# Kernel optimization log

Hardware: AMD Instinct MI355X
Metric: run time of the kernel (lower is better)

Reference implementation:

```python
import jax, jax.numpy as jnp
import numpy as np

B, S, D, H = 4, 2048, 1024, 16
HS = D // H  # head_size = 64


def setup_inputs() -> dict:
    key = jax.random.key(0)
    ks = jax.random.split(key, 6)
    scale = 1.0 / np.sqrt(D)
    return {
        "x": jax.random.normal(ks[0], (B, S, D), dtype=jnp.float32),
        "Wk": jax.random.normal(ks[1], (D, D), dtype=jnp.float32) * scale,
        "Wq": jax.random.normal(ks[2], (D, D), dtype=jnp.float32) * scale,
        "Wv": jax.random.normal(ks[3], (D, D), dtype=jnp.float32) * scale,
        "Wo": jax.random.normal(ks[4], (D, D), dtype=jnp.float32) * scale,
        "bo": jnp.zeros((D,), dtype=jnp.float32),
    }


def reference(x, Wk, Wq, Wv, Wo, bo):
    b, s, d = x.shape
    # torch nn.Linear: y = x @ W.T
    def heads(W):
        return (x @ W.T).reshape(b, s, H, HS).transpose(0, 2, 1, 3)  # [b,h,s,hs]
    k, q, v = heads(Wk), heads(Wq), heads(Wv)
    att = jnp.einsum("bhqd,bhkd->bhqk", q, k) * (1.0 / np.sqrt(HS))
    causal = jnp.tril(jnp.ones((s, s), dtype=bool))
    att = jnp.where(causal, att, -jnp.inf)
    att = jax.nn.softmax(att, axis=-1)
    # dropout in eval mode (identity) for deterministic reference
    out = jnp.einsum("bhqk,bhkd->bhqd", att, v)  # [b,h,s,hs]
    out = out.transpose(0, 2, 1, 3).reshape(b, s, d)
    return out @ Wo.T + bo
```

## Files before the change

kernel.cpp:

```cpp
#include <hip/hip_runtime.h>

#define B_ 4
#define S_ 2048
#define D_ 1024
#define H_ 16
#define HS_ 64

typedef float f32x4 __attribute__((ext_vector_type(4)));
typedef short bf16x8 __attribute__((ext_vector_type(8)));

__device__ inline short f2bf(float f) {
  union { float f; unsigned u; } v; v.f = f;
  unsigned r = v.u + 0x7fffu + ((v.u >> 16) & 1u);
  return (short)(r >> 16);
}
__device__ inline unsigned fbits(float f) {
  union { float f; unsigned u; } v; v.f = f; return v.u;
}

__device__ inline void load_lds16(const short* g, short* l) {
  __builtin_amdgcn_global_load_lds((const __attribute__((address_space(1))) void*)g,
                                   (__attribute__((address_space(3))) void*)l, 16, 0, 0);
}

__global__ __launch_bounds__(256) void cvt_f32_bf16(const float* __restrict__ in,
                                                    short* __restrict__ out, int n) {
  const int i = (blockIdx.x * 256 + threadIdx.x) * 4;
  if (i < n) {
    const float4 v = *(const float4*)(in + i);
    short4 o;
    o.x = f2bf(v.x); o.y = f2bf(v.y); o.z = f2bf(v.z); o.w = f2bf(v.w);
    *(short4*)(out + i) = o;
  }
}

__global__ __launch_bounds__(256) void cvt4_f32_bf16(const float* __restrict__ w0, const float* __restrict__ w1,
                                                     const float* __restrict__ w2, const float* __restrict__ w3,
                                                     short* __restrict__ o0, short* __restrict__ o1,
                                                     short* __restrict__ o2, short* __restrict__ o3, int n) {
  const float* in; short* out;
  switch (blockIdx.y) {
    case 0: in = w0; out = o0; break;
    case 1: in = w1; out = o1; break;
    case 2: in = w2; out = o2; break;
    default: in = w3; out = o3; break;
  }
  const int i = (blockIdx.x * 256 + threadIdx.x) * 4;
  if (i < n) {
    const float4 v = *(const float4*)(in + i);
    short4 o;
    o.x = f2bf(v.x); o.y = f2bf(v.y); o.z = f2bf(v.z); o.w = f2bf(v.w);
    *(short4*)(out + i) = o;
  }
}

__device__ inline void mfma_core(const short* lA, const short* lB, int wm, int wn,
                                 int col, int quad, f32x4 acc[4][4]) {
  bf16x8 af[4], bfr[4];
  for (int i = 0; i < 4; i++) af[i]  = *(const bf16x8*)&lA[(wm + i * 16 + col) * 32 + quad * 8];
  for (int j = 0; j < 4; j++) bfr[j] = *(const bf16x8*)&lB[(wn + j * 16 + col) * 32 + quad * 8];
  for (int i = 0; i < 4; i++)
    for (int j = 0; j < 4; j++)
      acc[i][j] = __builtin_amdgcn_mfma_f32_16x16x32_bf16(af[i], bfr[j], acc[i][j], 0, 0, 0);
}

template <bool CF32>
__global__ __launch_bounds__(256) void gemm_bb(const short* __restrict__ A,
                                               const short* __restrict__ Bt,
                                               void* __restrict__ Cv,
                                               const float* __restrict__ bias,
                                               int M, int N, int K) {
  __shared__ __align__(16) short lA[128 * 32];
  __shared__ __align__(16) short lB[128 * 32];
  const int tid = threadIdx.x;
  const int wave = tid >> 6, lane = tid & 63;
  const int quad = lane >> 4, col = lane & 15;
  const int m0 = blockIdx.x * 128, n0 = blockIdx.y * 128;
  const int wm = (wave >> 1) * 64, wn = (wave & 1) * 64;
  const int srow = wave * 32 + (lane >> 2);
  const int scol = (lane & 3) * 8;

  f32x4 acc[4][4];
  for (int i = 0; i < 4; i++)
    for (int j = 0; j < 4; j++) acc[i][j] = (f32x4){0.f, 0.f, 0.f, 0.f};

  for (int k0 = 0; k0 < K; k0 += 32) {
    __syncthreads();
    load_lds16(&A[(size_t)(m0 + srow) * K + k0 + scol],       &lA[srow * 32 + scol]);
    load_lds16(&A[(size_t)(m0 + srow + 16) * K + k0 + scol],  &lA[(srow + 16) * 32 + scol]);
    load_lds16(&Bt[(size_t)(n0 + srow) * K + k0 + scol],      &lB[srow * 32 + scol]);
    load_lds16(&Bt[(size_t)(n0 + srow + 16) * K + k0 + scol], &lB[(srow + 16) * 32 + scol]);
    __syncthreads();
    mfma_core(lA, lB, wm, wn, col, quad, acc);
  }

  for (int j = 0; j < 4; j++) {
    const int gn = n0 + wn + j * 16 + col;
    const float bv = bias ? bias[gn] : 0.f;
    for (int i = 0; i < 4; i++) {
      const int gm = m0 + wm + i * 16 + quad * 4;
      for (int r = 0; r < 4; r++) {
        if (CF32) ((float*)Cv)[(size_t)(gm + r) * N + gn] = acc[i][j][r] + bv;
        else      ((short*)Cv)[(size_t)(gm + r) * N + gn] = f2bf(acc[i][j][r] + bv);
      }
    }
  }
}

__global__ __launch_bounds__(256) void gemm_qkv(const short* __restrict__ A,
                                                const short* Wq, const short* Wk, const short* Wv,
                                                short* Cq, short* Ck, short* Cvt) {
  __shared__ __align__(16) short lA[128 * 32];
  __shared__ __align__(16) short lB[128 * 32];
  const int nsel = blockIdx.y >> 3;
  const int n0 = (blockIdx.y & 7) * 128;
  const short* Bt = nsel == 0 ? Wq : (nsel == 1 ? Wk : Wv);
  const int tid = threadIdx.x;
  const int wave = tid >> 6, lane = tid & 63;
  const int quad = lane >> 4, col = lane & 15;
  const int m0 = blockIdx.x * 128;
  const int wm = (wave >> 1) * 64, wn = (wave & 1) * 64;
  const int srow = wave * 32 + (lane >> 2);
  const int scol = (lane & 3) * 8;
  const int K = D_, N = D_;

  f32x4 acc[4][4];
  for (int i = 0; i < 4; i++)
    for (int j = 0; j < 4; j++) acc[i][j] = (f32x4){0.f, 0.f, 0.f, 0.f};

  for (int k0 = 0; k0 < K; k0 += 32) {
    __syncthreads();
    load_lds16(&A[(size_t)(m0 + srow) * K + k0 + scol],       &lA[srow * 32 + scol]);
    load_lds16(&A[(size_t)(m0 + srow + 16) * K + k0 + scol],  &lA[(srow + 16) * 32 + scol]);
    load_lds16(&Bt[(size_t)(n0 + srow) * K + k0 + scol],      &lB[srow * 32 + scol]);
    load_lds16(&Bt[(size_t)(n0 + srow + 16) * K + k0 + scol], &lB[(srow + 16) * 32 + scol]);
    __syncthreads();
    mfma_core(lA, lB, wm, wn, col, quad, acc);
  }

  if (nsel < 2) {
    short* C = nsel ? Ck : Cq;
    const float sc = nsel == 0 ? 0.18033688f : 1.0f;
    for (int j = 0; j < 4; j++) {
      const int gn = n0 + wn + j * 16 + col;
      for (int i = 0; i < 4; i++) {
        const int gm = m0 + wm + i * 16 + quad * 4;
        for (int r = 0; r < 4; r++)
          C[(size_t)(gm + r) * N + gn] = f2bf(acc[i][j][r] * sc);
      }
    }
  } else {
    for (int j = 0; j < 4; j++) {
      const int gn = n0 + wn + j * 16 + col;
      for (int i = 0; i < 4; i++) {
        const int gm = m0 + wm + i * 16 + quad * 4;
        const int bb = gm >> 11, s = gm & 2047;
        short4 o;
        o.x = f2bf(acc[i][j][0]); o.y = f2bf(acc[i][j][1]);
        o.z = f2bf(acc[i][j][2]); o.w = f2bf(acc[i][j][3]);
        *(short4*)&Cvt[((size_t)bb * D_ + gn) * (size_t)S_ + s] = o;
      }
    }
  }
}

__global__ __launch_bounds__(256) void flash_attn6(const short* __restrict__ Q,
                                                   const short* __restrict__ Kt,
                                                   const short* __restrict__ Vt,
                                                   short* __restrict__ O) {
  __shared__ __align__(16) short lK[2][64 * 64];
  __shared__ __align__(16) short lV[2][64 * 64];
  __shared__ __align__(16) short pl[4][16 * 64];
  const int tid = threadIdx.x, wave = tid >> 6, lane = tid & 63;
  const int quad = lane >> 4, col = lane & 15;
  const int bh = blockIdx.x;
  const int b = bh >> 4, h = bh & 15;
  const size_t qkbase = (size_t)b * S_ * D_ + (size_t)h * HS_;
  const size_t vtbase = ((size_t)b * D_ + (size_t)h * HS_) * (size_t)S_;

  const int srow = tid >> 3;
  const int scg = (tid & 7) ^ (srow & 7);
  const int cs0 = (quad ^ (col & 7)) * 8;
  const int cs1 = ((quad + 4) ^ (col & 7)) * 8;
  short* plw = pl[wave];

  bf16x8 ones;
  for (int i = 0; i < 8; i++) ones[i] = (short)0x3F80;

  int nb = 0;

  for (int half = 0; half < 2; half++) {
    const int s = half ? (int)blockIdx.y : 31 - (int)blockIdx.y;
    const int qmin = s * 64 + wave * 16;
    const int L = s;

    load_lds16(&Kt[qkbase + (size_t)srow * D_ + scg * 8],        &lK[nb][tid * 8]);
    load_lds16(&Kt[qkbase + (size_t)(32 + srow) * D_ + scg * 8], &lK[nb][2048 + tid * 8]);
    load_lds16(&Vt[vtbase + (size_t)srow * S_ + scg * 8],        &lV[nb][tid * 8]);
    load_lds16(&Vt[vtbase + (size_t)(srow + 32) * S_ + scg * 8], &lV[nb][2048 + tid * 8]);
    const int cur0 = nb;
    nb ^= 1;

    bf16x8 qf[2];
    for (int x = 0; x < 2; x++)
      qf[x] = *(const bf16x8*)&Q[qkbase + (size_t)(qmin + col) * D_ + x * 32 + quad * 8];

    f32x4 oacc[4], lacc;
    for (int dt = 0; dt < 4; dt++) oacc[dt] = (f32x4){0.f, 0.f, 0.f, 0.f};
    lacc = (f32x4){0.f, 0.f, 0.f, 0.f};

    for (int nt = 0; nt <= L; nt++) {
      const int n0 = nt * 64;
      const int cur = cur0 ^ (nt & 1);
      __syncthreads();
      if (nt < L) {
        const int nn = n0 + 64;
        load_lds16(&Kt[qkbase + (size_t)(nn + srow) * D_ + scg * 8],      &lK[nb][tid * 8]);
        load_lds16(&Kt[qkbase + (size_t)(nn + 32 + srow) * D_ + scg * 8], &lK[nb][2048 + tid * 8]);
        load_lds16(&Vt[vtbase + (size_t)srow * S_ + nn + scg * 8],        &lV[nb][tid * 8]);
        load_lds16(&Vt[vtbase + (size_t)(srow + 32) * S_ + nn + scg * 8], &lV[nb][2048 + tid * 8]);
        nb ^= 1;
      }

      const short* lKc = lK[cur];
      const short* lVc = lV[cur];
      const bool needM = (nt == L);

      bf16x8 kf[4][2];
      for (int t = 0; t < 4; t++) {
        const int rb = (t * 16 + col) * 64;
        kf[t][0] = *(const bf16x8*)&lKc[rb + cs0];
        kf[t][1] = *(const bf16x8*)&lKc[rb + cs1];
      }

      const int qg = qmin + col;
      for (int t = 0; t < 4; t++) {
        f32x4 z = (f32x4){0.f, 0.f, 0.f, 0.f};
        __builtin_amdgcn_s_setprio(1);
        z = __builtin_amdgcn_mfma_f32_16x16x32_bf16(kf[t][0], qf[0], z, 0, 0, 0);
        z = __builtin_amdgcn_mfma_f32_16x16x32_bf16(kf[t][1], qf[1], z, 0, 0, 0);
        __builtin_amdgcn_s_setprio(0);
        float p0 = exp2f(z[0]);
        float p1 = exp2f(z[1]);
        float p2 = exp2f(z[2]);
        float p3 = exp2f(z[3]);
        if (needM) {
          const int kv = n0 + t * 16 + quad * 4;
          if (kv + 0 > qg) p0 = 0.f;
          if (kv + 1 > qg) p1 = 0.f;
          if (kv + 2 > qg) p2 = 0.f;
          if (kv + 3 > qg) p3 = 0.f;
        }
        unsigned d0 = __builtin_amdgcn_perm(fbits(p1), fbits(p0), 0x07060302u);
        unsigned d1 = __builtin_amdgcn_perm(fbits(p3), fbits(p2), 0x07060302u);
        const int cc = (2 * t + (quad >> 1)) ^ (col & 7);
        uint2 w; w.x = d0; w.y = d1;
        *(uint2*)&plw[col * 64 + cc * 8 + (quad & 1) * 4] = w;
      }

      for (int h2 = 0; h2 < 2; h2++) {
        const int cgo = ((h2 * 4 + quad) ^ (col & 7)) * 8;
        const bf16x8 pf = *(const bf16x8*)&plw[col * 64 + cgo];
        bf16x8 vf[4];
        for (int dt = 0; dt < 4; dt++)
          vf[dt] = *(const bf16x8*)&lVc[(dt * 16 + col) * 64 + cgo];
        __builtin_amdgcn_s_setprio(1);
        lacc = __builtin_amdgcn_mfma_f32_16x16x32_bf16(pf, ones, lacc, 0, 0, 0);
        for (int dt = 0; dt < 4; dt++)
          oacc[dt] = __builtin_amdgcn_mfma_f32_16x16x32_bf16(pf, vf[dt], oacc[dt], 0, 0, 0);
        __builtin_amdgcn_s_setprio(0);
      }
    }

    for (int r = 0; r < 4; r++) {
      const float inv = 1.f / lacc[r];
      const size_t row = qkbase + (size_t)(qmin + quad * 4 + r) * D_;
      for (int dt = 0; dt < 4; dt++)
        O[row + dt * 16 + col] = f2bf(oacc[dt][r] * inv);
    }
  }
}

__global__ __launch_bounds__(256) void gemm_ff(const float* __restrict__ A,
                                               const float* __restrict__ Bt,
                                               short* __restrict__ C,
                                               int M, int N, int K) {
  __shared__ __align__(16) short lA[128 * 32];
  __shared__ __align__(16) short lB[128 * 32];
  const int tid = threadIdx.x;
  const int wave = tid >> 6, lane = tid & 63;
  const int quad = lane >> 4, col = lane & 15;
  const int m0 = blockIdx.y * 128, n0 = blockIdx.x * 128;
  const int wm = (wave >> 1) * 64, wn = (wave & 1) * 64;
  const int srow2 = tid >> 1;
  const int sc = (tid & 1) * 16;

  f32x4 acc[4][4];
  for (int i = 0; i < 4; i++)
    for (int j = 0; j < 4; j++) acc[i][j] = (f32x4){0.f, 0.f, 0.f, 0.f};

  for (int k0 = 0; k0 < K; k0 += 32) {
    __syncthreads();
    {
      const float4* ga = (const float4*)&A[(size_t)(m0 + srow2) * K + k0 + sc];
      const float4 v0 = ga[0], v1 = ga[1], v2 = ga[2], v3 = ga[3];
      bf16x8 p0, p1;
      p0[0] = f2bf(v0.x); p0[1] = f2bf(v0.y); p0[2] = f2bf(v0.z); p0[3] = f2bf(v0.w);
      p0[4] = f2bf(v1.x); p0[5] = f2bf(v1.y); p0[6] = f2bf(v1.z); p0[7] = f2bf(v1.w);
      p1[0] = f2bf(v2.x); p1[1] = f2bf(v2.y); p1[2] = f2bf(v2.z); p1[3] = f2bf(v2.w);
      p1[4] = f2bf(v3.x); p1[5] = f2bf(v3.y); p1[6] = f2bf(v3.z); p1[7] = f2bf(v3.w);
      *(bf16x8*)&lA[srow2 * 32 + sc]     = p0;
      *(bf16x8*)&lA[srow2 * 32 + sc + 8] = p1;
    }
    {
      const float4* gb = (const float4*)&Bt[(size_t)(n0 + srow2) * K + k0 + sc];
      const float4 v0 = gb[0], v1 = gb[1], v2 = gb[2], v3 = gb[3];
      bf16x8 p0, p1;
      p0[0] = f2bf(v0.x); p0[1] = f2bf(v0.y); p0[2] = f2bf(v0.z); p0[3] = f2bf(v0.w);
      p0[4] = f2bf(v1.x); p0[5] = f2bf(v1.y); p0[6] = f2bf(v1.z); p0[7] = f2bf(v1.w);
      p1[0] = f2bf(v2.x); p1[1] = f2bf(v2.y); p1[2] = f2bf(v2.z); p1[3] = f2bf(v2.w);
      p1[4] = f2bf(v3.x); p1[5] = f2bf(v3.y); p1[6] = f2bf(v3.z); p1[7] = f2bf(v3.w);
      *(bf16x8*)&lB[srow2 * 32 + sc]     = p0;
      *(bf16x8*)&lB[srow2 * 32 + sc + 8] = p1;
    }
    __syncthreads();
    mfma_core(lA, lB, wm, wn, col, quad, acc);
  }

  for (int j = 0; j < 4; j++) {
    const int gn = n0 + wn + j * 16 + col;
    for (int i = 0; i < 4; i++) {
      const int gm = m0 + wm + i * 16 + quad * 4;
      for (int r = 0; r < 4; r++)
        C[(size_t)(gm + r) * N + gn] = f2bf(acc[i][j][r]);
    }
  }
}

__global__ __launch_bounds__(256) void gemm_out_bf(const short* __restrict__ A,
                                                   const float* __restrict__ Bt,
                                                   float* __restrict__ C,
                                                   const float* __restrict__ bias,
                                                   int M, int N, int K) {
  __shared__ __align__(16) short lA[128 * 32];
  __shared__ __align__(16) short lB[128 * 32];
  const int tid = threadIdx.x;
  const int wave = tid >> 6, lane = tid & 63;
  const int quad = lane >> 4, col = lane & 15;
  const int m0 = blockIdx.y * 128, n0 = blockIdx.x * 128;
  const int wm = (wave >> 1) * 64, wn = (wave & 1) * 64;
  const int srow = wave * 32 + (lane >> 2);
  const int scol = (lane & 3) * 8;
  const int srow2 = tid >> 1;
  const int sc = (tid & 1) * 16;

  f32x4 acc[4][4];
  for (int i = 0; i < 4; i++)
    for (int j = 0; j < 4; j++) acc[i][j] = (f32x4){0.f, 0.f, 0.f, 0.f};

  for (int k0 = 0; k0 < K; k0 += 32) {
    __syncthreads();
    load_lds16(&A[(size_t)(m0 + srow) * K + k0 + scol],      &lA[srow * 32 + scol]);
    load_lds16(&A[(size_t)(m0 + srow + 16) * K + k0 + scol], &lA[(srow + 16) * 32 + scol]);
    {
      const float4* gb = (const float4*)&Bt[(size_t)(n0 + srow2) * K + k0 + sc];
      const float4 v0 = gb[0], v1 = gb[1], v2 = gb[2], v3 = gb[3];
      bf16x8 p0, p1;
      p0[0] = f2bf(v0.x); p0[1] = f2bf(v0.y); p0[2] = f2bf(v0.z); p0[3] = f2bf(v0.w);
      p0[4] = f2bf(v1.x); p0[5] = f2bf(v1.y); p0[6] = f2bf(v1.z); p0[7] = f2bf(v1.w);
      p1[0] = f2bf(v2.x); p1[1] = f2bf(v2.y); p1[2] = f2bf(v2.z); p1[3] = f2bf(v2.w);
      p1[4] = f2bf(v3.x); p1[5] = f2bf(v3.y); p1[6] = f2bf(v3.z); p1[7] = f2bf(v3.w);
      *(bf16x8*)&lB[srow2 * 32 + sc]     = p0;
      *(bf16x8*)&lB[srow2 * 32 + sc + 8] = p1;
    }
    __syncthreads();
    mfma_core(lA, lB, wm, wn, col, quad, acc);
  }

  for (int j = 0; j < 4; j++) {
    const int gn = n0 + wn + j * 16 + col;
    const float bv = bias ? bias[gn] : 0.f;
    for (int i = 0; i < 4; i++) {
      const int gm = m0 + wm + i * 16 + quad * 4;
      for (int r = 0; r < 4; r++)
        C[(size_t)(gm + r) * N + gn] = acc[i][j][r] + bv;
    }
  }
}

__global__ __launch_bounds__(64) void flash_attn(const short* __restrict__ Q,
                                                 const short* __restrict__ K,
                                                 const short* __restrict__ V,
                                                 short* __restrict__ O) {
  __shared__ __align__(16) short pl[16 * 40];
  const int lane = threadIdx.x;
  const int quad = lane >> 4, col = lane & 15;
  const int blk = blockIdx.x;
  const int qt = blk & 127;
  const int bh = blk >> 7;
  const int b = bh >> 4, h = bh & 15;
  const int q0 = qt * 16;
  const size_t base = (size_t)b * S_ * D_ + (size_t)h * HS_;

  const bf16x8 qf0 = *(const bf16x8*)&Q[base + (size_t)(q0 + col) * D_ + quad * 8];
  const bf16x8 qf1 = *(const bf16x8*)&Q[base + (size_t)(q0 + col) * D_ + 32 + quad * 8];

  float mr[4], lr[4];
  f32x4 oacc[4];
  for (int r = 0; r < 4; r++) { mr[r] = -1e30f; lr[r] = 0.f; }
  for (int dt = 0; dt < 4; dt++) oacc[dt] = (f32x4){0.f, 0.f, 0.f, 0.f};

  const int ntiles = (q0 + 15) / 32 + 1;
  for (int nt = 0; nt < ntiles; nt++) {
    const int n0 = nt * 32;
    f32x4 s[2];
    s[0] = (f32x4){0.f, 0.f, 0.f, 0.f};
    s[1] = (f32x4){0.f, 0.f, 0.f, 0.f};
    for (int t = 0; t < 2; t++) {
      const short* kp = &K[base + (size_t)(n0 + t * 16 + col) * D_ + quad * 8];
      const bf16x8 kf0 = *(const bf16x8*)kp;
      const bf16x8 kf1 = *(const bf16x8*)(kp + 32);
      s[t] = __builtin_amdgcn_mfma_f32_16x16x32_bf16(qf0, kf0, s[t], 0, 0, 0);
      s[t] = __builtin_amdgcn_mfma_f32_16x16x32_bf16(qf1, kf1, s[t], 0, 0, 0);
    }
    for (int r = 0; r < 4; r++) {
      const int mg = q0 + quad * 4 + r;
      float s0 = s[0][r] * 0.125f; if (n0 + col > mg)      s0 = -1e30f;
      float s1 = s[1][r] * 0.125f; if (n0 + 16 + col > mg) s1 = -1e30f;
      float tm = fmaxf(s0, s1);
      for (int off = 1; off < 16; off <<= 1) tm = fmaxf(tm, __shfl_xor(tm, off));
      const float mnew = fmaxf(mr[r], tm);
      const float alpha = __expf(mr[r] - mnew);
      mr[r] = mnew;
      const float p0 = __expf(s0 - mnew);
      const float p1 = __expf(s1 - mnew);
      float ps = p0 + p1;
      for (int off = 1; off < 16; off <<= 1) ps += __shfl_xor(ps, off);
      lr[r] = lr[r] * alpha + ps;
      for (int dt = 0; dt < 4; dt++) oacc[dt][r] *= alpha;
      pl[(quad * 4 + r) * 40 + col]      = f2bf(p0);
      pl[(quad * 4 + r) * 40 + 16 + col] = f2bf(p1);
    }
    const bf16x8 pf = *(const bf16x8*)&pl[col * 40 + quad * 8];
    for (int dt = 0; dt < 4; dt++) {
      bf16x8 vf;
      const short* vp = &V[base + (size_t)(n0 + quad * 8) * D_ + dt * 16 + col];
      for (int j = 0; j < 8; j++) vf[j] = vp[(size_t)j * D_];
      oacc[dt] = __builtin_amdgcn_mfma_f32_16x16x32_bf16(pf, vf, oacc[dt], 0, 0, 0);
    }
  }

  for (int r = 0; r < 4; r++) {
    const float inv = 1.f / lr[r];
    const size_t row = base + (size_t)(q0 + quad * 4 + r) * D_;
    for (int dt = 0; dt < 4; dt++)
      O[row + dt * 16 + col] = f2bf(oacc[dt][r] * inv);
  }
}

extern "C" void kernel_launch(void* const* d_in, const int* in_sizes, int n_in,
                              void* d_out, int out_size, void* d_ws, size_t ws_size,
                              hipStream_t stream) {
  const float* x  = (const float*)d_in[0];
  const float* Wk = (const float*)d_in[1];
  const float* Wq = (const float*)d_in[2];
  const float* Wv = (const float*)d_in[3];
  const float* Wo = (const float*)d_in[4];
  const float* bo = (const float*)d_in[5];
  float* out = (float*)d_out;

  char* ws = (char*)d_ws;
  const size_t MiB = 1u << 20;
  const int M = B_ * S_, N = D_, K = D_;
  const int nx = M * D_, nw = D_ * D_;

  if (ws_size >= 88 * MiB) {
    short* xb    = (short*)(ws);
    short* wkb   = (short*)(ws + 16 * MiB);
    short* wqb   = (short*)(ws + 18 * MiB);
    short* wvb   = (short*)(ws + 20 * MiB);
    short* wob   = (short*)(ws + 22 * MiB);
    short* q_ws  = (short*)(ws + 24 * MiB);
    short* k_ws  = (short*)(ws + 40 * MiB);
    short* vt_ws = (short*)(ws + 56 * MiB);
    short* a_ws  = (short*)(ws + 72 * MiB);

    hipLaunchKernelGGL(cvt_f32_bf16, dim3(nx / 1024), dim3(256), 0, stream, x, xb, nx);
    hipLaunchKernelGGL(cvt4_f32_bf16, dim3(nw / 1024, 4), dim3(256), 0, stream,
                       Wq, Wk, Wv, Wo, wqb, wkb, wvb, wob, nw);
    hipLaunchKernelGGL(gemm_qkv, dim3(M / 128, 24), dim3(256), 0, stream,
                       xb, wqb, wkb, wvb, q_ws, k_ws, vt_ws);
    hipLaunchKernelGGL(flash_attn6, dim3(B_ * H_, 16), dim3(256), 0, stream,
                       q_ws, k_ws, vt_ws, a_ws);
    hipLaunchKernelGGL((gemm_bb<true>), dim3(M / 128, N / 128), dim3(256), 0, stream,
                       a_ws, wob, (void*)out, bo, M, N, K);
  } else if (ws_size >= 64 * MiB) {
    short* q_ws = (short*)(ws);
    short* k_ws = (short*)(ws + 16 * MiB);
    short* v_ws = (short*)(ws + 32 * MiB);
    short* a_ws = (short*)(ws + 48 * MiB);
    dim3 gg(N / 128, M / 128), gb(256);
    hipLaunchKernelGGL(gemm_ff, gg, gb, 0, stream, x, Wq, q_ws, M, N, K);
    hipLaunchKernelGGL(gemm_ff, gg, gb, 0, stream, x, Wk, k_ws, M, N, K);
    hipLaunchKernelGGL(gemm_ff, gg, gb, 0, stream, x, Wv, v_ws, M, N, K);
    hipLaunchKernelGGL(flash_attn, dim3(B_ * H_ * (S_ / 16)), dim3(64), 0, stream, q_ws, k_ws, v_ws, a_ws);
    hipLaunchKernelGGL(gemm_out_bf, gg, gb, 0, stream, a_ws, Wo, out, bo, M, N, K);
  } else {
    short* q_ws = (short*)(ws);
    short* k_ws = (short*)(ws + 4 * MiB);
    short* v_ws = (short*)(ws + 8 * MiB);
    short* a_ws = (short*)(ws + 12 * MiB);
    const int Mb = S_;
    dim3 gg(N / 128, Mb / 128), gb(256);
    for (int b = 0; b < B_; b++) {
      const float* xb = x + (size_t)b * S_ * D_;
      float* ob = out + (size_t)b * S_ * D_;
      hipLaunchKernelGGL(gemm_ff, gg, gb, 0, stream, xb, Wq, q_ws, Mb, N, K);
      hipLaunchKernelGGL(gemm_ff, gg, gb, 0, stream, xb, Wk, k_ws, Mb, N, K);
      hipLaunchKernelGGL(gemm_ff, gg, gb, 0, stream, xb, Wv, v_ws, Mb, N, K);
      hipLaunchKernelGGL(flash_attn, dim3(H_ * (S_ / 16)), dim3(64), 0, stream, q_ws, k_ws, v_ws, a_ws);
      hipLaunchKernelGGL(gemm_out_bf, gg, gb, 0, stream, a_ws, Wo, ob, bo, Mb, N, K);
    }
  }
}
```

Measured before the change: 266.4 us.

## Double-buffer LDS with 64-wide K tiles and XOR swizzle in bf16 GEMMs

The bf16 GEMM kernels (gemm_bb and the fused QKV projection) now stage 128x64 K-tiles into two LDS buffers. The next tile is prefetched with global_load_lds while MFMAs run on the current one, so there is one barrier per iteration instead of two. An XOR swizzle on the LDS column groups is meant to avoid bank conflicts on the fragment reads. This raises LDS use to 64 KB per block, which may lower occupancy, and the kernels that convert fp32 on the fly keep the old single-buffer path with the MFMA loop inlined.

```diff
diff --git a/kernel.cpp b/kernel.cpp
--- a/kernel.cpp
+++ b/kernel.cpp
@@ -54,14 +54,26 @@
   }
 }
 
-__device__ inline void mfma_core(const short* lA, const short* lB, int wm, int wn,
-                                 int col, int quad, f32x4 acc[4][4]) {
-  bf16x8 af[4], bfr[4];
-  for (int i = 0; i < 4; i++) af[i]  = *(const bf16x8*)&lA[(wm + i * 16 + col) * 32 + quad * 8];
-  for (int j = 0; j < 4; j++) bfr[j] = *(const bf16x8*)&lB[(wn + j * 16 + col) * 32 + quad * 8];
-  for (int i = 0; i < 4; i++)
-    for (int j = 0; j < 4; j++)
-      acc[i][j] = __builtin_amdgcn_mfma_f32_16x16x32_bf16(af[i], bfr[j], acc[i][j], 0, 0, 0);
+__device__ inline void stage_tile64(const short* __restrict__ g, int ld, int k0,
+                                    short* l, int tid) {
+  const int srow = tid >> 3;
+  const int scol = (tid & 7) * 8;
+  const int scg  = ((tid & 7) ^ ((tid >> 3) & 7)) * 8;
+  for (int j = 0; j < 4; j++)
+    load_lds16(&g[(size_t)(srow + j * 32) * ld + k0 + scg], &l[(srow + j * 32) * 64 + scol]);
+}
+
+__device__ inline void mfma_core64(const short* lA, const short* lB, int wm, int wn,
+                                   int col, int quad, f32x4 acc[4][4]) {
+  for (int ks = 0; ks < 2; ks++) {
+    const int cs = ((ks * 4 + quad) ^ (col & 7)) * 8;
+    bf16x8 af[4], bfr[4];
+    for (int i = 0; i < 4; i++) af[i]  = *(const bf16x8*)&lA[(wm + i * 16 + col) * 64 + cs];
+    for (int j = 0; j < 4; j++) bfr[j] = *(const bf16x8*)&lB[(wn + j * 16 + col) * 64 + cs];
+    for (int i = 0; i < 4; i++)
+      for (int j = 0; j < 4; j++)
+        acc[i][j] = __builtin_amdgcn_mfma_f32_16x16x32_bf16(af[i], bfr[j], acc[i][j], 0, 0, 0);
+  }
 }
 
 template <bool CF32>
@@ -70,28 +82,30 @@
                                                void* __restrict__ Cv,
                                                const float* __restrict__ bias,
                                                int M, int N, int K) {
-  __shared__ __align__(16) short lA[128 * 32];
-  __shared__ __align__(16) short lB[128 * 32];
+  __shared__ __align__(16) short lA[2][128 * 64];
+  __shared__ __align__(16) short lB[2][128 * 64];
   const int tid = threadIdx.x;
   const int wave = tid >> 6, lane = tid & 63;
   const int quad = lane >> 4, col = lane & 15;
   const int m0 = blockIdx.x * 128, n0 = blockIdx.y * 128;
   const int wm = (wave >> 1) * 64, wn = (wave & 1) * 64;
-  const int srow = wave * 32 + (lane >> 2);
-  const int scol = (lane & 3) * 8;
 
   f32x4 acc[4][4];
   for (int i = 0; i < 4; i++)
     for (int j = 0; j < 4; j++) acc[i][j] = (f32x4){0.f, 0.f, 0.f, 0.f};
 
-  for (int k0 = 0; k0 < K; k0 += 32) {
+  const int NT = K >> 6;
+  stage_tile64(&A[(size_t)m0 * K], K, 0, lA[0], tid);
+  stage_tile64(&Bt[(size_t)n0 * K], K, 0, lB[0], tid);
+  __syncthreads();
+  for (int kt = 0; kt < NT; kt++) {
+    const int cur = kt & 1;
+    if (kt + 1 < NT) {
+      stage_tile64(&A[(size_t)m0 * K], K, (kt + 1) * 64, lA[cur ^ 1], tid);
+      stage_tile64(&Bt[(size_t)n0 * K], K, (kt + 1) * 64, lB[cur ^ 1], tid);
+    }
+    mfma_core64(lA[cur], lB[cur], wm, wn, col, quad, acc);
     __syncthreads();
-    load_lds16(&A[(size_t)(m0 + srow) * K + k0 + scol],       &lA[srow * 32 + scol]);
-    load_lds16(&A[(size_t)(m0 + srow + 16) * K + k0 + scol],  &lA[(srow + 16) * 32 + scol]);
-    load_lds16(&Bt[(size_t)(n0 + srow) * K + k0 + scol],      &lB[srow * 32 + scol]);
-    load_lds16(&Bt[(size_t)(n0 + srow + 16) * K + k0 + scol], &lB[(srow + 16) * 32 + scol]);
-    __syncthreads();
-    mfma_core(lA, lB, wm, wn, col, quad, acc);
   }
 
   for (int j = 0; j < 4; j++) {
@@ -110,8 +124,8 @@
 __global__ __launch_bounds__(256) void gemm_qkv(const short* __restrict__ A,
                                                 const short* Wq, const short* Wk, const short* Wv,
                                                 short* Cq, short* Ck, short* Cvt) {
-  __shared__ __align__(16) short lA[128 * 32];
-  __shared__ __align__(16) short lB[128 * 32];
+  __shared__ __align__(16) short lA[2][128 * 64];
+  __shared__ __align__(16) short lB[2][128 * 64];
   const int nsel = blockIdx.y >> 3;
   const int n0 = (blockIdx.y & 7) * 128;
   const short* Bt = nsel == 0 ? Wq : (nsel == 1 ? Wk : Wv);
@@ -120,22 +134,24 @@
   const int quad = lane >> 4, col = lane & 15;
   const int m0 = blockIdx.x * 128;
   const int wm = (wave >> 1) * 64, wn = (wave & 1) * 64;
-  const int srow = wave * 32 + (lane >> 2);
-  const int scol = (lane & 3) * 8;
   const int K = D_, N = D_;
 
   f32x4 acc[4][4];
   for (int i = 0; i < 4; i++)
     for (int j = 0; j < 4; j++) acc[i][j] = (f32x4){0.f, 0.f, 0.f, 0.f};
 
-  for (int k0 = 0; k0 < K; k0 += 32) {
+  const int NT = K >> 6;
+  stage_tile64(&A[(size_t)m0 * K], K, 0, lA[0], tid);
+  stage_tile64(&Bt[(size_t)n0 * K], K, 0, lB[0], tid);
+  __syncthreads();
+  for (int kt = 0; kt < NT; kt++) {
+    const int cur = kt & 1;
+    if (kt + 1 < NT) {
+      stage_tile64(&A[(size_t)m0 * K], K, (kt + 1) * 64, lA[cur ^ 1], tid);
+      stage_tile64(&Bt[(size_t)n0 * K], K, (kt + 1) * 64, lB[cur ^ 1], tid);
+    }
+    mfma_core64(lA[cur], lB[cur], wm, wn, col, quad, acc);
     __syncthreads();
-    load_lds16(&A[(size_t)(m0 + srow) * K + k0 + scol],       &lA[srow * 32 + scol]);
-    load_lds16(&A[(size_t)(m0 + srow + 16) * K + k0 + scol],  &lA[(srow + 16) * 32 + scol]);
-    load_lds16(&Bt[(size_t)(n0 + srow) * K + k0 + scol],      &lB[srow * 32 + scol]);
-    load_lds16(&Bt[(size_t)(n0 + srow + 16) * K + k0 + scol], &lB[(srow + 16) * 32 + scol]);
-    __syncthreads();
-    mfma_core(lA, lB, wm, wn, col, quad, acc);
   }
 
   if (nsel < 2) {
@@ -324,7 +340,14 @@
       *(bf16x8*)&lB[srow2 * 32 + sc + 8] = p1;
     }
     __syncthreads();
-    mfma_core(lA, lB, wm, wn, col, quad, acc);
+    {
+      bf16x8 af[4], bfr[4];
+      for (int i = 0; i < 4; i++) af[i]  = *(const bf16x8*)&lA[(wm + i * 16 + col) * 32 + quad * 8];
+      for (int j = 0; j < 4; j++) bfr[j] = *(const bf16x8*)&lB[(wn + j * 16 + col) * 32 + quad * 8];
+      for (int i = 0; i < 4; i++)
+        for (int j = 0; j < 4; j++)
+          acc[i][j] = __builtin_amdgcn_mfma_f32_16x16x32_bf16(af[i], bfr[j], acc[i][j], 0, 0, 0);
+    }
   }
 
   for (int j = 0; j < 4; j++) {
@@ -374,7 +397,14 @@
       *(bf16x8*)&lB[srow2 * 32 + sc + 8] = p1;
     }
     __syncthreads();
-    mfma_core(lA, lB, wm, wn, col, quad, acc);
+    {
+      bf16x8 af[4], bfr[4];
+      for (int i = 0; i < 4; i++) af[i]  = *(const bf16x8*)&lA[(wm + i * 16 + col) * 32 + quad * 8];
+      for (int j = 0; j < 4; j++) bfr[j] = *(const bf16x8*)&lB[(wn + j * 16 + col) * 32 + quad * 8];
+      for (int i = 0; i < 4; i++)
+        for (int j = 0; j < 4; j++)
+          acc[i][j] = __builtin_amdgcn_mfma_f32_16x16x32_bf16(af[i], bfr[j], acc[i][j], 0, 0, 0);
+    }
   }
 
   for (int j = 0; j < 4; j++) {
```

Measured after the change: 267.4 us. Within noise of the previous version (+0.4%).
